# Kernel tuning notes

Measured on AMD Instinct MI355X. Metric: run time of the kernel, lower is better.

The kernel has to match this reference:

```python
import jax, jax.numpy as jnp
import numpy as np

N, E, D, L = 50000, 250000, 300, 5
ATOM_V, BOND_V = 128, 16
BN_EPS = 1e-5


def setup_inputs() -> dict:
    key = jax.random.key(0)
    ks = jax.random.split(key, 16)
    inp = {
        'x': jax.random.randint(ks[0], (N, 9), 0, ATOM_V),
        'edge_index': jax.random.randint(ks[1], (2, E), 0, N),
        'edge_attr': jax.random.randint(ks[2], (E, 3), 0, BOND_V),
        # learned parameters
        'atom_emb': jax.random.normal(ks[3], (9, ATOM_V, D), jnp.float32) * 0.02,
        'bond_emb': jax.random.normal(ks[4], (L, 3, BOND_V, D), jnp.float32) * 0.02,
        'eps': jnp.zeros((L,), jnp.float32),
        'W1': jax.random.normal(ks[5], (L, D, 2 * D), jnp.float32) / np.sqrt(D),
        'b1': jnp.zeros((L, 2 * D), jnp.float32),
        'g1': jnp.ones((L, 2 * D), jnp.float32),
        'be1': jnp.zeros((L, 2 * D), jnp.float32),
        'W2': jax.random.normal(ks[6], (L, 2 * D, D), jnp.float32) / np.sqrt(2 * D),
        'b2': jnp.zeros((L, D), jnp.float32),
        'gamma': jnp.ones((L, D), jnp.float32),
        'beta': jnp.zeros((L, D), jnp.float32),
    }
    return inp


def _bn(h, g, b):
    m = h.mean(0)
    v = h.var(0)
    return (h - m) * jax.lax.rsqrt(v + BN_EPS) * g + b


def reference(x, edge_index, edge_attr, atom_emb, bond_emb, eps, W1, b1, g1, be1, W2, b2, gamma, beta):
    src, dst = edge_index[0], edge_index[1]
    # AtomEncoder: sum of per-column embeddings -> [N, D]
    h = atom_emb[jnp.arange(9)[:, None], x.T].sum(0)
    for l in range(L):
        # BondEncoder for this layer -> [E, D]
        e = bond_emb[l][jnp.arange(3)[:, None], edge_attr.T].sum(0)
        # GIN: gather -> relu message -> scatter-add
        msg = jax.nn.relu(h[src] + e)
        agg = jax.ops.segment_sum(msg, dst, num_segments=N)
        z = (1.0 + eps[l]) * h + agg
        # MLP: Linear -> BN -> ReLU -> Linear
        z = jax.nn.relu(_bn(z @ W1[l] + b1[l], g1[l], be1[l])) @ W2[l] + b2[l]
        # outer BatchNorm
        h = _bn(z, gamma[l], beta[l])
        if l < L - 1:
            h = jax.nn.relu(h)
    return h  # JK='last'
```

## Files before the change

kernel.cpp:

```cpp
#include <hip/hip_runtime.h>

#define N_NODES 50000
#define N_EDGES 250000
#define DIM 300
#define DIM2 600
#define NL 5
#define MPAD 50048
#define KP1 320
#define KP2 608
#define NP1 640
#define NP2 384
#define SCAN_BLOCKS 196
#define CT_STRIDE 136

typedef __attribute__((ext_vector_type(8))) _Float16 half8;
typedef __attribute__((ext_vector_type(2))) _Float16 half2v;
typedef __attribute__((ext_vector_type(8))) short short8;
typedef __attribute__((ext_vector_type(4))) float f32x4;
typedef unsigned short ushort;
typedef unsigned int uint;

#define AS1 __attribute__((address_space(1)))
#define AS3 __attribute__((address_space(3)))

static __device__ __forceinline__ ushort f2h(float f) {
    _Float16 h = (_Float16)f;
    return __builtin_bit_cast(ushort, h);
}
static __device__ __forceinline__ float h2f(ushort s) {
    return (float)__builtin_bit_cast(_Float16, s);
}
static __device__ __forceinline__ uint pk2(float a, float b) {
    return (uint)f2h(a) | ((uint)f2h(b) << 16);
}
static __device__ __forceinline__ half2v u2h2(uint u) {
    return __builtin_bit_cast(half2v, u);
}

__global__ void atom_enc(const int* __restrict__ x, const float* __restrict__ emb,
                         ushort* __restrict__ h) {
    int idx = blockIdx.x * blockDim.x + threadIdx.x;
    const int PAIRS = DIM / 2;
    if (idx >= N_NODES * PAIRS) return;
    int n = idx / PAIRS, p = idx - n * PAIRS;
    const int* xr = x + n * 9;
    float s0 = 0.f, s1 = 0.f;
#pragma unroll
    for (int i = 0; i < 9; i++) {
        const float2 v = *(const float2*)(emb + (size_t)(i * 128 + xr[i]) * DIM + 2 * p);
        s0 += v.x; s1 += v.y;
    }
    ((uint*)h)[idx] = pk2(s0, s1);
}

__global__ void deg_count(const int* __restrict__ ei, int* __restrict__ deg) {
    int e = blockIdx.x * blockDim.x + threadIdx.x;
    if (e < N_EDGES) atomicAdd(&deg[ei[N_EDGES + e]], 1);
}

__global__ void block_sums(const int* __restrict__ deg, int* __restrict__ bsum) {
    __shared__ int red[256];
    int tid = threadIdx.x;
    int node = blockIdx.x * 256 + tid;
    red[tid] = (node < N_NODES) ? deg[node] : 0;
    __syncthreads();
    for (int off = 128; off > 0; off >>= 1) {
        if (tid < off) red[tid] += red[tid + off];
        __syncthreads();
    }
    if (tid == 0) bsum[blockIdx.x] = red[0];
}

__global__ void scan_bsums(int* __restrict__ bsum) {
    __shared__ int s[256];
    int tid = threadIdx.x;
    int orig = (tid < SCAN_BLOCKS) ? bsum[tid] : 0;
    s[tid] = orig;
    __syncthreads();
    for (int off = 1; off < 256; off <<= 1) {
        int v = (tid >= off) ? s[tid - off] : 0;
        __syncthreads();
        s[tid] += v;
        __syncthreads();
    }
    if (tid < SCAN_BLOCKS) bsum[tid] = s[tid] - orig;
}

__global__ void write_rowstart(const int* __restrict__ deg, const int* __restrict__ bsum,
                               int* __restrict__ rowstart, int* __restrict__ cursor) {
    __shared__ int s[256];
    int tid = threadIdx.x;
    int node = blockIdx.x * 256 + tid;
    int d = (node < N_NODES) ? deg[node] : 0;
    s[tid] = d;
    __syncthreads();
    for (int off = 1; off < 256; off <<= 1) {
        int v = (tid >= off) ? s[tid - off] : 0;
        __syncthreads();
        s[tid] += v;
        __syncthreads();
    }
    int excl = s[tid] - d + bsum[blockIdx.x];
    if (node < N_NODES) {
        rowstart[node] = excl;
        cursor[node] = excl;
    }
    if (blockIdx.x == 0 && tid == 0) rowstart[N_NODES] = N_EDGES;
}

__global__ void csr_fill(const int* __restrict__ ei, const int* __restrict__ ea,
                         int* __restrict__ cursor, int2* __restrict__ epack) {
    int e = blockIdx.x * blockDim.x + threadIdx.x;
    if (e < N_EDGES) {
        int d = ei[N_EDGES + e];
        int slot = atomicAdd(&cursor[d], 1);
        int attr = ea[3 * e] | (ea[3 * e + 1] << 8) | (ea[3 * e + 2] << 16);
        epack[slot] = make_int2(ei[e], attr);
    }
}

__global__ void bond_conv(const float* __restrict__ bond, ushort* __restrict__ bondh) {
    int idx = blockIdx.x * blockDim.x + threadIdx.x;
    if (idx >= 48 * (DIM / 2)) return;
    float2 v = *(const float2*)(bond + 2 * idx);
    ((uint*)bondh)[idx] = pk2(v.x, v.y);
}

__global__ void init_bn(float* __restrict__ scale, float* __restrict__ shift) {
    int i = blockIdx.x * blockDim.x + threadIdx.x;
    if (i < DIM) { scale[i] = 1.f; shift[i] = 0.f; }
}

__launch_bounds__(256)
__global__ void agg_combine(const int* __restrict__ rowstart, const int2* __restrict__ epack,
                            const ushort* __restrict__ bondh, const ushort* __restrict__ h,
                            const float* __restrict__ scale, const float* __restrict__ shift,
                            int relu, const float* __restrict__ epsp, int layer,
                            ushort* __restrict__ A1) {
    int node = blockIdx.x * 4 + (threadIdx.x >> 6);
    int lane = threadIdx.x & 63;
    if (node >= MPAD) return;
    uint* row32 = (uint*)(A1 + (size_t)node * KP1);
    if (node >= N_NODES) {
        for (int i = lane; i < KP1 / 2; i += 64) row32[i] = 0;
        return;
    }
    const int PAIRS = DIM / 2;
    float2 scf[3], shf[3];
    half2v sch[3], shh[3];
#pragma unroll
    for (int i = 0; i < 3; i++) {
        int p = lane + 64 * i;
        scf[i] = make_float2(0.f, 0.f);
        shf[i] = make_float2(0.f, 0.f);
        if (p < PAIRS) {
            scf[i] = *(const float2*)(scale + 2 * p);
            shf[i] = *(const float2*)(shift + 2 * p);
        }
        sch[i] = half2v{(_Float16)scf[i].x, (_Float16)scf[i].y};
        shh[i] = half2v{(_Float16)shf[i].x, (_Float16)shf[i].y};
    }
    float epsv = 1.0f + epsp[layer];
    const uint* hd = (const uint*)(h + (size_t)node * DIM);
    float ax[3], ay[3];
#pragma unroll
    for (int i = 0; i < 3; i++) {
        int p = lane + 64 * i;
        ax[i] = 0.f; ay[i] = 0.f;
        if (p < PAIRS) {
            uint u = hd[p];
            float vx = h2f((ushort)(u & 0xffffu)) * scf[i].x + shf[i].x;
            float vy = h2f((ushort)(u >> 16)) * scf[i].y + shf[i].y;
            if (relu) { vx = fmaxf(vx, 0.f); vy = fmaxf(vy, 0.f); }
            ax[i] = epsv * vx; ay[i] = epsv * vy;
        }
    }

    auto edge_contrib = [&](int2 pk) {
        const uint* hs = (const uint*)(h + (size_t)pk.x * DIM);
        int a0 = pk.y & 0xff, a1v = (pk.y >> 8) & 0xff, a2 = (pk.y >> 16) & 0xff;
        const uint* t0 = (const uint*)(bondh + a0 * DIM);
        const uint* t1 = (const uint*)(bondh + (16 + a1v) * DIM);
        const uint* t2 = (const uint*)(bondh + (32 + a2) * DIM);
        const half2v z = {};
#pragma unroll
        for (int i = 0; i < 3; i++) {
            int p = lane + 64 * i;
            if (p < PAIRS) {
                half2v hv = u2h2(hs[p]) * sch[i] + shh[i];
                if (relu) hv = __builtin_elementwise_max(hv, z);
                half2v m = hv + u2h2(t0[p]) + u2h2(t1[p]) + u2h2(t2[p]);
                m = __builtin_elementwise_max(m, z);
                ax[i] += (float)m.x;
                ay[i] += (float)m.y;
            }
        }
    };

    int e0 = rowstart[node], e1 = rowstart[node + 1];
    int t = e0;
    for (; t + 1 < e1; t += 2) {
        int2 p0 = epack[t];
        int2 p1 = epack[t + 1];
        edge_contrib(p0);
        edge_contrib(p1);
    }
    if (t < e1) edge_contrib(epack[t]);

#pragma unroll
    for (int i = 0; i < 3; i++) {
        int p = lane + 64 * i;
        if (p < KP1 / 2) row32[p] = (p < PAIRS) ? pk2(ax[i], ay[i]) : 0u;
    }
}

__global__ void wt_conv(const float* __restrict__ W, ushort* __restrict__ Wt,
                        int K, int Nc, int KP, int NP) {
    int idx = blockIdx.x * blockDim.x + threadIdx.x;
    if (idx >= KP * NP) return;
    int k = idx / NP, n = idx - k * NP;
    ushort v = 0;
    if (k < K && n < Nc) v = f2h(W[(size_t)k * Nc + n]);
    Wt[(size_t)n * KP + k] = v;
}

__global__ void wt_conv2(const float* __restrict__ W, const float* __restrict__ scale,
                         ushort* __restrict__ Wt) {
    int idx = blockIdx.x * blockDim.x + threadIdx.x;
    if (idx >= KP2 * NP2) return;
    int k = idx / NP2, n = idx - k * NP2;
    ushort v = 0;
    if (k < DIM2 && n < DIM) v = f2h(scale[k] * W[(size_t)k * DIM + n]);
    Wt[(size_t)n * KP2 + k] = v;
}

__launch_bounds__(256)
__global__ void gemm_mfma(const ushort* __restrict__ A, const ushort* __restrict__ Wt,
                          const float* __restrict__ bias, ushort* __restrict__ Cout,
                          int M, int KP, int Nc, int strideC, int ntiles,
                          float* __restrict__ csum, float* __restrict__ csq) {
    __shared__ ushort smem[128 * CT_STRIDE];
    __shared__ float s_sum[128], s_sq[128];
    ushort* As = smem;
    ushort* Bs = smem + 4096;

    int tid = threadIdx.x;
    int w = tid >> 6, lane = tid & 63;
    int quad = lane >> 4, lr = lane & 15;
    int wm = w >> 1, wn = w & 1;
    int bx = blockIdx.x;
    int m0 = (bx / ntiles) * 128;
    int n0 = (bx % ntiles) * 128;

    if (tid < 128) { s_sum[tid] = 0.f; s_sq[tid] = 0.f; }

    f32x4 acc[4][4] = {};
    int kq = lane & 3;

    for (int k0 = 0; k0 < KP; k0 += 32) {
#pragma unroll
        for (int c = w; c < 8; c += 4) {
            int row = 16 * c + (lane >> 2);
            const ushort* gp = A + (size_t)(m0 + row) * KP + k0 + kq * 8;
            __builtin_amdgcn_global_load_lds((const AS1 void*)gp, (AS3 void*)(As + c * 512), 16, 0, 0);
        }
#pragma unroll
        for (int c = w; c < 8; c += 4) {
            int row = 16 * c + (lane >> 2);
            const ushort* gp = Wt + (size_t)(n0 + row) * KP + k0 + kq * 8;
            __builtin_amdgcn_global_load_lds((const AS1 void*)gp, (AS3 void*)(Bs + c * 512), 16, 0, 0);
        }
        __syncthreads();

        half8 a[4], b[4];
#pragma unroll
        for (int mf = 0; mf < 4; mf++)
            a[mf] = __builtin_bit_cast(half8, *(const short8*)(As + (64 * wm + 16 * mf + lr) * 32 + quad * 8));
#pragma unroll
        for (int nf = 0; nf < 4; nf++)
            b[nf] = __builtin_bit_cast(half8, *(const short8*)(Bs + (64 * wn + 16 * nf + lr) * 32 + quad * 8));
#pragma unroll
        for (int mf = 0; mf < 4; mf++)
#pragma unroll
            for (int nf = 0; nf < 4; nf++)
                acc[mf][nf] = __builtin_amdgcn_mfma_f32_16x16x32_f16(a[mf], b[nf], acc[mf][nf], 0, 0, 0);
        __syncthreads();
    }

#pragma unroll
    for (int nf = 0; nf < 4; nf++) {
        int lcol = 64 * wn + 16 * nf + lr;
        int gn = n0 + lcol;
        float bv = (gn < Nc) ? bias[gn] : 0.f;
        float ps = 0.f, pq = 0.f;
#pragma unroll
        for (int mf = 0; mf < 4; mf++) {
#pragma unroll
            for (int r = 0; r < 4; r++) {
                int lrow = 64 * wm + 16 * mf + quad * 4 + r;
                float v = acc[mf][nf][r] + bv;
                smem[lrow * CT_STRIDE + lcol] = f2h(v);
                if (m0 + lrow < M && gn < Nc) { ps += v; pq += v * v; }
            }
        }
        if (gn < Nc) {
            atomicAdd(&s_sum[lcol], ps);
            atomicAdd(&s_sq[lcol], pq);
        }
    }
    __syncthreads();

#pragma unroll
    for (int it = 0; it < 8; it++) {
        int idx = tid + it * 256;
        int row = idx >> 4, ch = idx & 15;
        int gcol = n0 + ch * 8;
        if (gcol < Nc) {
            *(short8*)(Cout + (size_t)(m0 + row) * strideC + gcol) =
                *(const short8*)(smem + row * CT_STRIDE + ch * 8);
        }
    }

    if (tid < 128) {
        int gn = n0 + tid;
        if (gn < Nc) {
            atomicAdd(&csum[gn], s_sum[tid]);
            atomicAdd(&csq[gn], s_sq[tid]);
        }
    }
}

__launch_bounds__(256)
__global__ void gemm2_fused(const ushort* __restrict__ yh, const ushort* __restrict__ Wt,
                            const ushort* __restrict__ t1h, const float* __restrict__ bias,
                            ushort* __restrict__ hout,
                            float* __restrict__ csum, float* __restrict__ csq) {
    __shared__ ushort smem[128 * CT_STRIDE];
    __shared__ ushort s_t[KP2];
    __shared__ float s_sum[128], s_sq[128];
    ushort* As = smem;
    ushort* Bs = smem + 4096;

    int tid = threadIdx.x;
    int w = tid >> 6, lane = tid & 63;
    int quad = lane >> 4, lr = lane & 15;
    int wm = w >> 1, wn = w & 1;
    int bx = blockIdx.x;
    int m0 = (bx / 3) * 128;
    int n0 = (bx % 3) * 128;

    for (int i = tid; i < KP2 / 2; i += 256) ((uint*)s_t)[i] = ((const uint*)t1h)[i];
    if (tid < 128) { s_sum[tid] = 0.f; s_sq[tid] = 0.f; }
    __syncthreads();

    f32x4 acc[4][4] = {};
    int kq = lane & 3;
    int cc = (tid & 3) * 8;
    int r0 = tid >> 2;

    for (int k0 = 0; k0 < KP2; k0 += 32) {
#pragma unroll
        for (int c = w; c < 8; c += 4) {
            int row = 16 * c + (lane >> 2);
            const ushort* gp = Wt + (size_t)(n0 + row) * KP2 + k0 + kq * 8;
            __builtin_amdgcn_global_load_lds((const AS1 void*)gp, (AS3 void*)(Bs + c * 512), 16, 0, 0);
        }
        int col = k0 + cc;
        short8 v0, v1;
        if (col < DIM2) {
            half8 t = *(const half8*)(s_t + col);
            half8 y0 = *(const half8*)(yh + (size_t)(m0 + r0) * DIM2 + col);
            half8 y1 = *(const half8*)(yh + (size_t)(m0 + r0 + 64) * DIM2 + col);
            half8 z = {};
            y0 = __builtin_elementwise_max(y0 + t, z);
            y1 = __builtin_elementwise_max(y1 + t, z);
            v0 = __builtin_bit_cast(short8, y0);
            v1 = __builtin_bit_cast(short8, y1);
        } else {
            v0 = short8{}; v1 = short8{};
        }
        *(short8*)(As + r0 * 32 + cc) = v0;
        *(short8*)(As + (r0 + 64) * 32 + cc) = v1;
        __syncthreads();

        half8 a[4], b[4];
#pragma unroll
        for (int mf = 0; mf < 4; mf++)
            a[mf] = __builtin_bit_cast(half8, *(const short8*)(As + (64 * wm + 16 * mf + lr) * 32 + quad * 8));
#pragma unroll
        for (int nf = 0; nf < 4; nf++)
            b[nf] = __builtin_bit_cast(half8, *(const short8*)(Bs + (64 * wn + 16 * nf + lr) * 32 + quad * 8));
#pragma unroll
        for (int mf = 0; mf < 4; mf++)
#pragma unroll
            for (int nf = 0; nf < 4; nf++)
                acc[mf][nf] = __builtin_amdgcn_mfma_f32_16x16x32_f16(a[mf], b[nf], acc[mf][nf], 0, 0, 0);
        __syncthreads();
    }

#pragma unroll
    for (int nf = 0; nf < 4; nf++) {
        int lcol = 64 * wn + 16 * nf + lr;
        int gn = n0 + lcol;
        float bv = (gn < DIM) ? bias[gn] : 0.f;
        float ps = 0.f, pq = 0.f;
#pragma unroll
        for (int mf = 0; mf < 4; mf++) {
#pragma unroll
            for (int r = 0; r < 4; r++) {
                int lrow = 64 * wm + 16 * mf + quad * 4 + r;
                float v = acc[mf][nf][r] + bv;
                smem[lrow * CT_STRIDE + lcol] = f2h(v);
                if (m0 + lrow < N_NODES && gn < DIM) { ps += v; pq += v * v; }
            }
        }
        if (gn < DIM) {
            atomicAdd(&s_sum[lcol], ps);
            atomicAdd(&s_sq[lcol], pq);
        }
    }
    __syncthreads();

#pragma unroll
    for (int it = 0; it < 16; it++) {
        int idx = tid + it * 256;
        int row = idx >> 5, ch = idx & 31;
        int gm = m0 + row, gcol = n0 + ch * 4;
        if (gm < N_NODES && gcol < DIM) {
            *(uint2*)(hout + (size_t)gm * DIM + gcol) =
                *(const uint2*)(smem + row * CT_STRIDE + ch * 4);
        }
    }

    if (tid < 128) {
        int gn = n0 + tid;
        if (gn < DIM) {
            atomicAdd(&csum[gn], s_sum[tid]);
            atomicAdd(&csq[gn], s_sq[tid]);
        }
    }
}

__global__ void bn_finalize(const float* __restrict__ sum, const float* __restrict__ sq,
                            const float* __restrict__ g, const float* __restrict__ b,
                            float* __restrict__ scale, float* __restrict__ shift,
                            ushort* __restrict__ th, int n, int npad) {
    int i = blockIdx.x * blockDim.x + threadIdx.x;
    if (i >= n) {
        if (th && i < npad) th[i] = 0;
        return;
    }
    const float invN = 1.0f / (float)N_NODES;
    float m = sum[i] * invN;
    float v = sq[i] * invN - m * m;
    float inv = rsqrtf(v + 1e-5f);
    float sc = g[i] * inv;
    scale[i] = sc;
    shift[i] = b[i] - m * sc;
    if (th) th[i] = f2h((b[i] - m * sc) / sc);
}

__global__ void bn_apply_out(const ushort* __restrict__ h, const float* __restrict__ scale,
                             const float* __restrict__ shift, float* __restrict__ out) {
    int idx = blockIdx.x * blockDim.x + threadIdx.x;
    const int PAIRS = DIM / 2;
    if (idx >= N_NODES * PAIRS) return;
    int p = idx % PAIRS;
    uint u = ((const uint*)h)[idx];
    float2 sc = *(const float2*)(scale + 2 * p);
    float2 sh = *(const float2*)(shift + 2 * p);
    float2 o;
    o.x = h2f((ushort)(u & 0xffffu)) * sc.x + sh.x;
    o.y = h2f((ushort)(u >> 16)) * sc.y + sh.y;
    *(float2*)(out + 2 * idx) = o;
}

extern "C" void kernel_launch(void* const* d_in, const int* in_sizes, int n_in,
                              void* d_out, int out_size, void* d_ws, size_t ws_size,
                              hipStream_t stream) {
    const int* x = (const int*)d_in[0];
    const int* ei = (const int*)d_in[1];
    const int* ea = (const int*)d_in[2];
    const float* atom_emb = (const float*)d_in[3];
    const float* bond_emb = (const float*)d_in[4];
    const float* eps = (const float*)d_in[5];
    const float* W1 = (const float*)d_in[6];
    const float* b1 = (const float*)d_in[7];
    const float* g1 = (const float*)d_in[8];
    const float* be1 = (const float*)d_in[9];
    const float* W2 = (const float*)d_in[10];
    const float* b2 = (const float*)d_in[11];
    const float* gamma = (const float*)d_in[12];
    const float* beta = (const float*)d_in[13];
    float* out = (float*)d_out;

    float* ws = (float*)d_ws;
    ushort* h    = (ushort*)ws;
    ushort* A1h  = (ushort*)(ws + 7500000);
    ushort* yh   = (ushort*)(ws + 15507680);
    ushort* Wt1  = (ushort*)(ws + 30522080);
    ushort* Wt2  = (ushort*)(ws + 30624480);
    ushort* bondh = (ushort*)(ws + 30741216);
    float* stats = ws + 30748416;
    ushort* t1h  = (ushort*)(ws + 30752016);
    int* rowstart = (int*)(ws + 30752320);
    int* deg      = rowstart + 50001;
    int* cursor   = deg + 50000;
    int2* epack   = (int2*)(cursor + 50000 + 1);
    int* bsum     = (int*)(epack + 250000);

    float* sum1 = stats;
    float* sq1  = stats + 600;
    float* sum2 = stats + 1200;
    float* sq2  = stats + 1500;
    float* scale1 = stats + 1800;
    float* shift1 = stats + 2400;
    float* scale2 = stats + 3000;
    float* shift2 = stats + 3300;

    const int PAIRS_N = N_NODES * (DIM / 2);

    hipMemsetAsync(deg, 0, 50000 * sizeof(int), stream);
    deg_count<<<(N_EDGES + 255) / 256, 256, 0, stream>>>(ei, deg);
    block_sums<<<SCAN_BLOCKS, 256, 0, stream>>>(deg, bsum);
    scan_bsums<<<1, 256, 0, stream>>>(bsum);
    write_rowstart<<<SCAN_BLOCKS, 256, 0, stream>>>(deg, bsum, rowstart, cursor);
    csr_fill<<<(N_EDGES + 255) / 256, 256, 0, stream>>>(ei, ea, cursor, epack);

    atom_enc<<<(PAIRS_N + 255) / 256, 256, 0, stream>>>(x, atom_emb, h);
    init_bn<<<(DIM + 255) / 256, 256, 0, stream>>>(scale2, shift2);

    for (int l = 0; l < NL; ++l) {
        hipMemsetAsync(stats, 0, 1800 * sizeof(float), stream);

        bond_conv<<<(48 * (DIM / 2) + 255) / 256, 256, 0, stream>>>(
            bond_emb + (size_t)l * 3 * 16 * DIM, bondh);

        agg_combine<<<(MPAD + 3) / 4, 256, 0, stream>>>(rowstart, epack, bondh,
                                                        h, scale2, shift2, (l > 0) ? 1 : 0,
                                                        eps, l, A1h);

        wt_conv<<<(KP1 * NP1 + 255) / 256, 256, 0, stream>>>(W1 + (size_t)l * DIM * DIM2, Wt1,
                                                             DIM, DIM2, KP1, NP1);

        gemm_mfma<<<(MPAD / 128) * (NP1 / 128), 256, 0, stream>>>(
            A1h, Wt1, b1 + l * DIM2, yh, N_NODES, KP1, DIM2, DIM2, NP1 / 128, sum1, sq1);

        bn_finalize<<<(KP2 + 255) / 256, 256, 0, stream>>>(sum1, sq1, g1 + l * DIM2,
                                                           be1 + l * DIM2, scale1, shift1,
                                                           t1h, DIM2, KP2);

        wt_conv2<<<(KP2 * NP2 + 255) / 256, 256, 0, stream>>>(W2 + (size_t)l * DIM2 * DIM,
                                                              scale1, Wt2);

        gemm2_fused<<<(MPAD / 128) * (NP2 / 128), 256, 0, stream>>>(
            yh, Wt2, t1h, b2 + l * DIM, h, sum2, sq2);

        bn_finalize<<<(DIM + 255) / 256, 256, 0, stream>>>(sum2, sq2, gamma + l * DIM,
                                                           beta + l * DIM, scale2, shift2,
                                                           nullptr, DIM, DIM);
    }

    bn_apply_out<<<(PAIRS_N + 255) / 256, 256, 0, stream>>>(h, scale2, shift2, out);
}
```

Before: 1.195 ms.

## Double-buffer GEMM LDS tiles with XOR swizzle and XCD-aware block remap

Both MFMA GEMM kernels now double-buffer their LDS tiles. The global-to-LDS load for the next k-step is issued before the current step's MFMAs, so there is one barrier per step instead of two. LDS columns are XOR-swizzled to avoid bank conflicts on the 128-bit reads, block IDs are remapped so neighbouring tiles land on the same XCD for L2 reuse, and MFMA bursts are raised in priority. This uses twice the tile LDS inside the existing smem array and relies on hand-placed waitcnt and barriers, which are fragile to get right.

After: 1.108 ms. 7.3% less time.

```diff
diff --git a/kernel.cpp b/kernel.cpp
--- a/kernel.cpp
+++ b/kernel.cpp
@@ -35,6 +35,18 @@
 }
 static __device__ __forceinline__ half2v u2h2(uint u) {
     return __builtin_bit_cast(half2v, u);
+}
+
+static __device__ __forceinline__ short8 lds_read_b128(uint addr) {
+    short8 r;
+    asm volatile("ds_read_b128 %0, %1" : "=v"(r) : "v"(addr));
+    return r;
+}
+
+static __device__ __forceinline__ int xcd_swizzle(int o, int nwg) {
+    int q = nwg >> 3, r = nwg & 7;
+    int xcd = o & 7, idx = o >> 3;
+    return (xcd < r ? xcd * (q + 1) : r * (q + 1) + (xcd - r) * q) + idx;
 }
 
 __global__ void atom_enc(const int* __restrict__ x, const float* __restrict__ emb,
@@ -241,50 +253,74 @@
                           float* __restrict__ csum, float* __restrict__ csq) {
     __shared__ ushort smem[128 * CT_STRIDE];
     __shared__ float s_sum[128], s_sq[128];
-    ushort* As = smem;
-    ushort* Bs = smem + 4096;
 
     int tid = threadIdx.x;
     int w = tid >> 6, lane = tid & 63;
     int quad = lane >> 4, lr = lane & 15;
     int wm = w >> 1, wn = w & 1;
-    int bx = blockIdx.x;
-    int m0 = (bx / ntiles) * 128;
-    int n0 = (bx % ntiles) * 128;
+    int wg = xcd_swizzle(blockIdx.x, gridDim.x);
+    int m0 = (wg / ntiles) * 128;
+    int n0 = (wg % ntiles) * 128;
 
     if (tid < 128) { s_sum[tid] = 0.f; s_sq[tid] = 0.f; }
 
+    const int kchunk = ((lane & 3) ^ ((lane >> 3) & 3)) * 8;
+    const int grow = lane >> 2;
+    const ushort* Abase = A + (size_t)m0 * KP + kchunk;
+    const ushort* Bbase = Wt + (size_t)n0 * KP + kchunk;
+
+    const uint sbase = (uint)(size_t)(AS3 ushort*)smem;
+    const int xq = (quad ^ ((lr >> 1) & 3)) * 8;
+    uint aoff[4], boff[4];
+#pragma unroll
+    for (int mf = 0; mf < 4; mf++)
+        aoff[mf] = sbase + (uint)(((64 * wm + 16 * mf + lr) * 32 + xq) * 2);
+#pragma unroll
+    for (int nf = 0; nf < 4; nf++)
+        boff[nf] = sbase + (uint)((4096 + (64 * wn + 16 * nf + lr) * 32 + xq) * 2);
+
+    auto stage = [&](int k0, int buf) {
+        ushort* dA = smem + buf * 8192;
+#pragma unroll
+        for (int c = w; c < 8; c += 4)
+            __builtin_amdgcn_global_load_lds((const AS1 void*)(Abase + (size_t)(16 * c + grow) * KP + k0),
+                                             (AS3 void*)(dA + c * 512), 16, 0, 0);
+#pragma unroll
+        for (int c = w; c < 8; c += 4)
+            __builtin_amdgcn_global_load_lds((const AS1 void*)(Bbase + (size_t)(16 * c + grow) * KP + k0),
+                                             (AS3 void*)(dA + 4096 + c * 512), 16, 0, 0);
+    };
+
     f32x4 acc[4][4] = {};
-    int kq = lane & 3;
-
-    for (int k0 = 0; k0 < KP; k0 += 32) {
-#pragma unroll
-        for (int c = w; c < 8; c += 4) {
-            int row = 16 * c + (lane >> 2);
-            const ushort* gp = A + (size_t)(m0 + row) * KP + k0 + kq * 8;
-            __builtin_amdgcn_global_load_lds((const AS1 void*)gp, (AS3 void*)(As + c * 512), 16, 0, 0);
-        }
-#pragma unroll
-        for (int c = w; c < 8; c += 4) {
-            int row = 16 * c + (lane >> 2);
-            const ushort* gp = Wt + (size_t)(n0 + row) * KP + k0 + kq * 8;
-            __builtin_amdgcn_global_load_lds((const AS1 void*)gp, (AS3 void*)(Bs + c * 512), 16, 0, 0);
-        }
-        __syncthreads();
-
-        half8 a[4], b[4];
+    const int nk = KP >> 5;
+
+    stage(0, 0);
+    asm volatile("s_waitcnt vmcnt(0) lgkmcnt(0)" ::: "memory");
+    __builtin_amdgcn_s_barrier();
+
+    for (int t = 0; t < nk; ++t) {
+        uint bsel = (uint)(t & 1) * 16384u;
+        if (t + 1 < nk) stage((t + 1) << 5, (t & 1) ^ 1);
+
+        short8 a[4], b[4];
+#pragma unroll
+        for (int mf = 0; mf < 4; mf++) a[mf] = lds_read_b128(aoff[mf] + bsel);
+#pragma unroll
+        for (int nf = 0; nf < 4; nf++) b[nf] = lds_read_b128(boff[nf] + bsel);
+        asm volatile("s_waitcnt lgkmcnt(0)" ::: "memory");
+        __builtin_amdgcn_sched_barrier(0);
+        __builtin_amdgcn_s_setprio(1);
 #pragma unroll
         for (int mf = 0; mf < 4; mf++)
-            a[mf] = __builtin_bit_cast(half8, *(const short8*)(As + (64 * wm + 16 * mf + lr) * 32 + quad * 8));
-#pragma unroll
-        for (int nf = 0; nf < 4; nf++)
-            b[nf] = __builtin_bit_cast(half8, *(const short8*)(Bs + (64 * wn + 16 * nf + lr) * 32 + quad * 8));
-#pragma unroll
-        for (int mf = 0; mf < 4; mf++)
 #pragma unroll
             for (int nf = 0; nf < 4; nf++)
-                acc[mf][nf] = __builtin_amdgcn_mfma_f32_16x16x32_f16(a[mf], b[nf], acc[mf][nf], 0, 0, 0);
-        __syncthreads();
+                acc[mf][nf] = __builtin_amdgcn_mfma_f32_16x16x32_f16(
+                    __builtin_bit_cast(half8, a[mf]), __builtin_bit_cast(half8, b[nf]),
+                    acc[mf][nf], 0, 0, 0);
+        __builtin_amdgcn_s_setprio(0);
+
+        asm volatile("s_waitcnt vmcnt(0)" ::: "memory");
+        __builtin_amdgcn_s_barrier();
     }
 
 #pragma unroll
@@ -338,64 +374,114 @@
     __shared__ ushort smem[128 * CT_STRIDE];
     __shared__ ushort s_t[KP2];
     __shared__ float s_sum[128], s_sq[128];
-    ushort* As = smem;
-    ushort* Bs = smem + 4096;
 
     int tid = threadIdx.x;
     int w = tid >> 6, lane = tid & 63;
     int quad = lane >> 4, lr = lane & 15;
     int wm = w >> 1, wn = w & 1;
-    int bx = blockIdx.x;
-    int m0 = (bx / 3) * 128;
-    int n0 = (bx % 3) * 128;
-
+    int wg = xcd_swizzle(blockIdx.x, gridDim.x);
+    int m0 = (wg / 3) * 128;
+    int n0 = (wg % 3) * 128;
+
+    int r0 = tid >> 2;
+    int q = tid & 3;
+    int cc = q * 8;
+    const int aslot = (q ^ ((r0 >> 1) & 3)) * 8;
+
+    const uint sbase = (uint)(size_t)(AS3 ushort*)smem;
+    const int xq = (quad ^ ((lr >> 1) & 3)) * 8;
+    uint aoff[4], boff[4];
+#pragma unroll
+    for (int mf = 0; mf < 4; mf++)
+        aoff[mf] = sbase + (uint)(((64 * wm + 16 * mf + lr) * 32 + xq) * 2);
+#pragma unroll
+    for (int nf = 0; nf < 4; nf++)
+        boff[nf] = sbase + (uint)((4096 + (64 * wn + 16 * nf + lr) * 32 + xq) * 2);
+
+    const int kchunk = ((lane & 3) ^ ((lane >> 3) & 3)) * 8;
+    const int grow = lane >> 2;
+    const ushort* Bbase = Wt + (size_t)n0 * KP2 + kchunk;
+
+    auto stageB = [&](int k0, int buf) {
+        ushort* dB = smem + buf * 8192 + 4096;
+#pragma unroll
+        for (int c = w; c < 8; c += 4)
+            __builtin_amdgcn_global_load_lds((const AS1 void*)(Bbase + (size_t)(16 * c + grow) * KP2 + k0),
+                                             (AS3 void*)(dB + c * 512), 16, 0, 0);
+    };
+
+    const ushort* yrow0 = yh + (size_t)(m0 + r0) * DIM2 + cc;
+    const ushort* yrow1 = yh + (size_t)(m0 + r0 + 64) * DIM2 + cc;
+
+    if (tid < 128) { s_sum[tid] = 0.f; s_sq[tid] = 0.f; }
+
+    half8 y0 = *(const half8*)(yrow0);
+    half8 y1 = *(const half8*)(yrow1);
+    stageB(0, 0);
     for (int i = tid; i < KP2 / 2; i += 256) ((uint*)s_t)[i] = ((const uint*)t1h)[i];
-    if (tid < 128) { s_sum[tid] = 0.f; s_sq[tid] = 0.f; }
     __syncthreads();
+    {
+        half8 z = {};
+        half8 tt = *(const half8*)(s_t + cc);
+        half8 a0 = __builtin_elementwise_max(y0 + tt, z);
+        half8 a1 = __builtin_elementwise_max(y1 + tt, z);
+        *(short8*)(smem + r0 * 32 + aslot) = __builtin_bit_cast(short8, a0);
+        *(short8*)(smem + (r0 + 64) * 32 + aslot) = __builtin_bit_cast(short8, a1);
+    }
+    asm volatile("s_waitcnt lgkmcnt(0)" ::: "memory");
+    __builtin_amdgcn_s_barrier();
 
     f32x4 acc[4][4] = {};
-    int kq = lane & 3;
-    int cc = (tid & 3) * 8;
-    int r0 = tid >> 2;
-
-    for (int k0 = 0; k0 < KP2; k0 += 32) {
-#pragma unroll
-        for (int c = w; c < 8; c += 4) {
-            int row = 16 * c + (lane >> 2);
-            const ushort* gp = Wt + (size_t)(n0 + row) * KP2 + k0 + kq * 8;
-            __builtin_amdgcn_global_load_lds((const AS1 void*)gp, (AS3 void*)(Bs + c * 512), 16, 0, 0);
-        }
-        int col = k0 + cc;
-        short8 v0, v1;
-        if (col < DIM2) {
-            half8 t = *(const half8*)(s_t + col);
-            half8 y0 = *(const half8*)(yh + (size_t)(m0 + r0) * DIM2 + col);
-            half8 y1 = *(const half8*)(yh + (size_t)(m0 + r0 + 64) * DIM2 + col);
+    const int nk = KP2 >> 5;
+
+    for (int t = 0; t < nk; ++t) {
+        uint bsel = (uint)(t & 1) * 16384u;
+        int nxt = (t & 1) ^ 1;
+        half8 yn0 = {}, yn1 = {};
+        int coln = ((t + 1) << 5) + cc;
+        int vn = 0;
+        if (t + 1 < nk) {
+            vn = coln < DIM2;
+            if (vn) {
+                yn0 = *(const half8*)(yrow0 + ((t + 1) << 5));
+                yn1 = *(const half8*)(yrow1 + ((t + 1) << 5));
+            }
+            stageB((t + 1) << 5, nxt);
+        }
+
+        short8 a[4], b[4];
+#pragma unroll
+        for (int mf = 0; mf < 4; mf++) a[mf] = lds_read_b128(aoff[mf] + bsel);
+#pragma unroll
+        for (int nf = 0; nf < 4; nf++) b[nf] = lds_read_b128(boff[nf] + bsel);
+        asm volatile("s_waitcnt lgkmcnt(0)" ::: "memory");
+        __builtin_amdgcn_sched_barrier(0);
+        __builtin_amdgcn_s_setprio(1);
+#pragma unroll
+        for (int mf = 0; mf < 4; mf++)
+#pragma unroll
+            for (int nf = 0; nf < 4; nf++)
+                acc[mf][nf] = __builtin_amdgcn_mfma_f32_16x16x32_f16(
+                    __builtin_bit_cast(half8, a[mf]), __builtin_bit_cast(half8, b[nf]),
+                    acc[mf][nf], 0, 0, 0);
+        __builtin_amdgcn_s_setprio(0);
+        __builtin_amdgcn_sched_barrier(0);
+
+        if (t + 1 < nk) {
+            ushort* Anx = smem + nxt * 8192;
             half8 z = {};
-            y0 = __builtin_elementwise_max(y0 + t, z);
-            y1 = __builtin_elementwise_max(y1 + t, z);
-            v0 = __builtin_bit_cast(short8, y0);
-            v1 = __builtin_bit_cast(short8, y1);
-        } else {
-            v0 = short8{}; v1 = short8{};
-        }
-        *(short8*)(As + r0 * 32 + cc) = v0;
-        *(short8*)(As + (r0 + 64) * 32 + cc) = v1;
-        __syncthreads();
-
-        half8 a[4], b[4];
-#pragma unroll
-        for (int mf = 0; mf < 4; mf++)
-            a[mf] = __builtin_bit_cast(half8, *(const short8*)(As + (64 * wm + 16 * mf + lr) * 32 + quad * 8));
-#pragma unroll
-        for (int nf = 0; nf < 4; nf++)
-            b[nf] = __builtin_bit_cast(half8, *(const short8*)(Bs + (64 * wn + 16 * nf + lr) * 32 + quad * 8));
-#pragma unroll
-        for (int mf = 0; mf < 4; mf++)
-#pragma unroll
-            for (int nf = 0; nf < 4; nf++)
-                acc[mf][nf] = __builtin_amdgcn_mfma_f32_16x16x32_f16(a[mf], b[nf], acc[mf][nf], 0, 0, 0);
-        __syncthreads();
+            half8 a0 = z, a1 = z;
+            if (vn) {
+                half8 tt = *(const half8*)(s_t + coln);
+                a0 = __builtin_elementwise_max(yn0 + tt, z);
+                a1 = __builtin_elementwise_max(yn1 + tt, z);
+            }
+            *(short8*)(Anx + r0 * 32 + aslot) = __builtin_bit_cast(short8, a0);
+            *(short8*)(Anx + (r0 + 64) * 32 + aslot) = __builtin_bit_cast(short8, a1);
+        }
+
+        asm volatile("s_waitcnt vmcnt(0) lgkmcnt(0)" ::: "memory");
+        __builtin_amdgcn_s_barrier();
     }
 
 #pragma unroll
```

## Swizzle LDS, halve epilogue smem, XCD-swizzle blocks, raise GEMM occupancy

Applied to the files above, without the earlier changes.

Both GEMM kernels now write the C tile back through shared memory in two 64-row halves, which halves the LDS buffer and, together with launch_bounds(256,6), lets more workgroups fit per CU. The shared-memory tiles use an XOR swizzle on the 8-element k-chunk to reduce bank conflicts in the MFMA operand reads. Block indices are remapped across the 8 XCDs so neighbouring tiles share L2, and s_setprio raises wave priority around the MFMA block. The costs are an extra pair of barriers in the epilogue and possible register pressure from the occupancy hint.

After: 3.143 ms. 2.63x slower.

```diff
diff --git a/kernel.cpp b/kernel.cpp
--- a/kernel.cpp
+++ b/kernel.cpp
@@ -35,6 +35,12 @@
 }
 static __device__ __forceinline__ half2v u2h2(uint u) {
     return __builtin_bit_cast(half2v, u);
+}
+
+static __device__ __forceinline__ int xcd_swizzle(int o, int nwg) {
+    int q = nwg >> 3, r = nwg & 7;
+    int xcd = o & 7, idx = o >> 3;
+    return (xcd < r ? xcd * (q + 1) : r * (q + 1) + (xcd - r) * q) + idx;
 }
 
 __global__ void atom_enc(const int* __restrict__ x, const float* __restrict__ emb,
@@ -234,12 +240,12 @@
     Wt[(size_t)n * KP2 + k] = v;
 }
 
-__launch_bounds__(256)
+__launch_bounds__(256, 6)
 __global__ void gemm_mfma(const ushort* __restrict__ A, const ushort* __restrict__ Wt,
                           const float* __restrict__ bias, ushort* __restrict__ Cout,
                           int M, int KP, int Nc, int strideC, int ntiles,
                           float* __restrict__ csum, float* __restrict__ csq) {
-    __shared__ ushort smem[128 * CT_STRIDE];
+    __shared__ ushort smem[64 * CT_STRIDE];
     __shared__ float s_sum[128], s_sq[128];
     ushort* As = smem;
     ushort* Bs = smem + 4096;
@@ -248,77 +254,85 @@
     int w = tid >> 6, lane = tid & 63;
     int quad = lane >> 4, lr = lane & 15;
     int wm = w >> 1, wn = w & 1;
-    int bx = blockIdx.x;
-    int m0 = (bx / ntiles) * 128;
-    int n0 = (bx % ntiles) * 128;
+    int wg = xcd_swizzle(blockIdx.x, gridDim.x);
+    int m0 = (wg / ntiles) * 128;
+    int n0 = (wg % ntiles) * 128;
 
     if (tid < 128) { s_sum[tid] = 0.f; s_sq[tid] = 0.f; }
 
+    const int kchunk = ((lane & 3) ^ ((lane >> 3) & 3)) * 8;
+    const int grow = lane >> 2;
+    const ushort* Abase = A + (size_t)m0 * KP + kchunk;
+    const ushort* Bbase = Wt + (size_t)n0 * KP + kchunk;
+    const int xq = (quad ^ ((lr >> 1) & 3)) * 8;
+
     f32x4 acc[4][4] = {};
-    int kq = lane & 3;
 
     for (int k0 = 0; k0 < KP; k0 += 32) {
 #pragma unroll
-        for (int c = w; c < 8; c += 4) {
-            int row = 16 * c + (lane >> 2);
-            const ushort* gp = A + (size_t)(m0 + row) * KP + k0 + kq * 8;
-            __builtin_amdgcn_global_load_lds((const AS1 void*)gp, (AS3 void*)(As + c * 512), 16, 0, 0);
-        }
-#pragma unroll
-        for (int c = w; c < 8; c += 4) {
-            int row = 16 * c + (lane >> 2);
-            const ushort* gp = Wt + (size_t)(n0 + row) * KP + k0 + kq * 8;
-            __builtin_amdgcn_global_load_lds((const AS1 void*)gp, (AS3 void*)(Bs + c * 512), 16, 0, 0);
-        }
+        for (int c = w; c < 8; c += 4)
+            __builtin_amdgcn_global_load_lds((const AS1 void*)(Abase + (size_t)(16 * c + grow) * KP + k0),
+                                             (AS3 void*)(As + c * 512), 16, 0, 0);
+#pragma unroll
+        for (int c = w; c < 8; c += 4)
+            __builtin_amdgcn_global_load_lds((const AS1 void*)(Bbase + (size_t)(16 * c + grow) * KP + k0),
+                                             (AS3 void*)(Bs + c * 512), 16, 0, 0);
         __syncthreads();
 
         half8 a[4], b[4];
 #pragma unroll
         for (int mf = 0; mf < 4; mf++)
-            a[mf] = __builtin_bit_cast(half8, *(const short8*)(As + (64 * wm + 16 * mf + lr) * 32 + quad * 8));
+            a[mf] = __builtin_bit_cast(half8, *(const short8*)(As + (64 * wm + 16 * mf + lr) * 32 + xq));
 #pragma unroll
         for (int nf = 0; nf < 4; nf++)
-            b[nf] = __builtin_bit_cast(half8, *(const short8*)(Bs + (64 * wn + 16 * nf + lr) * 32 + quad * 8));
+            b[nf] = __builtin_bit_cast(half8, *(const short8*)(Bs + (64 * wn + 16 * nf + lr) * 32 + xq));
+        __builtin_amdgcn_s_setprio(1);
 #pragma unroll
         for (int mf = 0; mf < 4; mf++)
 #pragma unroll
             for (int nf = 0; nf < 4; nf++)
                 acc[mf][nf] = __builtin_amdgcn_mfma_f32_16x16x32_f16(a[mf], b[nf], acc[mf][nf], 0, 0, 0);
-        __syncthreads();
-    }
-
-#pragma unroll
-    for (int nf = 0; nf < 4; nf++) {
-        int lcol = 64 * wn + 16 * nf + lr;
-        int gn = n0 + lcol;
-        float bv = (gn < Nc) ? bias[gn] : 0.f;
-        float ps = 0.f, pq = 0.f;
-#pragma unroll
-        for (int mf = 0; mf < 4; mf++) {
-#pragma unroll
-            for (int r = 0; r < 4; r++) {
-                int lrow = 64 * wm + 16 * mf + quad * 4 + r;
-                float v = acc[mf][nf][r] + bv;
-                smem[lrow * CT_STRIDE + lcol] = f2h(v);
-                if (m0 + lrow < M && gn < Nc) { ps += v; pq += v * v; }
+        __builtin_amdgcn_s_setprio(0);
+        __syncthreads();
+    }
+
+#pragma unroll
+    for (int half = 0; half < 2; half++) {
+        if (wm == half) {
+#pragma unroll
+            for (int nf = 0; nf < 4; nf++) {
+                int lcol = 64 * wn + 16 * nf + lr;
+                int gn = n0 + lcol;
+                float bv = (gn < Nc) ? bias[gn] : 0.f;
+                float ps = 0.f, pq = 0.f;
+#pragma unroll
+                for (int mf = 0; mf < 4; mf++) {
+#pragma unroll
+                    for (int r = 0; r < 4; r++) {
+                        int lrow = 16 * mf + quad * 4 + r;
+                        float v = acc[mf][nf][r] + bv;
+                        smem[lrow * CT_STRIDE + lcol] = f2h(v);
+                        if (m0 + 64 * half + lrow < M && gn < Nc) { ps += v; pq += v * v; }
+                    }
+                }
+                if (gn < Nc) {
+                    atomicAdd(&s_sum[lcol], ps);
+                    atomicAdd(&s_sq[lcol], pq);
+                }
             }
         }
-        if (gn < Nc) {
-            atomicAdd(&s_sum[lcol], ps);
-            atomicAdd(&s_sq[lcol], pq);
-        }
-    }
-    __syncthreads();
-
-#pragma unroll
-    for (int it = 0; it < 8; it++) {
-        int idx = tid + it * 256;
-        int row = idx >> 4, ch = idx & 15;
-        int gcol = n0 + ch * 8;
-        if (gcol < Nc) {
-            *(short8*)(Cout + (size_t)(m0 + row) * strideC + gcol) =
-                *(const short8*)(smem + row * CT_STRIDE + ch * 8);
-        }
+        __syncthreads();
+#pragma unroll
+        for (int it = 0; it < 4; it++) {
+            int idx = tid + it * 256;
+            int row = idx >> 4, ch = idx & 15;
+            int gcol = n0 + ch * 8;
+            if (gcol < Nc) {
+                *(short8*)(Cout + (size_t)(m0 + 64 * half + row) * strideC + gcol) =
+                    *(const short8*)(smem + row * CT_STRIDE + ch * 8);
+            }
+        }
+        __syncthreads();
     }
 
     if (tid < 128) {
@@ -330,12 +344,12 @@
     }
 }
 
-__launch_bounds__(256)
+__launch_bounds__(256, 6)
 __global__ void gemm2_fused(const ushort* __restrict__ yh, const ushort* __restrict__ Wt,
                             const ushort* __restrict__ t1h, const float* __restrict__ bias,
                             ushort* __restrict__ hout,
                             float* __restrict__ csum, float* __restrict__ csq) {
-    __shared__ ushort smem[128 * CT_STRIDE];
+    __shared__ ushort smem[64 * CT_STRIDE];
     __shared__ ushort s_t[KP2];
     __shared__ float s_sum[128], s_sq[128];
     ushort* As = smem;
@@ -345,91 +359,104 @@
     int w = tid >> 6, lane = tid & 63;
     int quad = lane >> 4, lr = lane & 15;
     int wm = w >> 1, wn = w & 1;
-    int bx = blockIdx.x;
-    int m0 = (bx / 3) * 128;
-    int n0 = (bx % 3) * 128;
-
+    int wg = xcd_swizzle(blockIdx.x, gridDim.x);
+    int m0 = (wg / 3) * 128;
+    int n0 = (wg % 3) * 128;
+
+    int r0 = tid >> 2;
+    int q = tid & 3;
+    int cc = q * 8;
+    const int aslot = (q ^ ((r0 >> 1) & 3)) * 8;
+
+    const int kchunk = ((lane & 3) ^ ((lane >> 3) & 3)) * 8;
+    const int grow = lane >> 2;
+    const ushort* Bbase = Wt + (size_t)n0 * KP2 + kchunk;
+    const int xq = (quad ^ ((lr >> 1) & 3)) * 8;
+
+    const ushort* yrow0 = yh + (size_t)(m0 + r0) * DIM2 + cc;
+    const ushort* yrow1 = yh + (size_t)(m0 + r0 + 64) * DIM2 + cc;
+
+    if (tid < 128) { s_sum[tid] = 0.f; s_sq[tid] = 0.f; }
     for (int i = tid; i < KP2 / 2; i += 256) ((uint*)s_t)[i] = ((const uint*)t1h)[i];
-    if (tid < 128) { s_sum[tid] = 0.f; s_sq[tid] = 0.f; }
     __syncthreads();
 
     f32x4 acc[4][4] = {};
-    int kq = lane & 3;
-    int cc = (tid & 3) * 8;
-    int r0 = tid >> 2;
-
-    for (int k0 = 0; k0 < KP2; k0 += 32) {
-#pragma unroll
-        for (int c = w; c < 8; c += 4) {
-            int row = 16 * c + (lane >> 2);
-            const ushort* gp = Wt + (size_t)(n0 + row) * KP2 + k0 + kq * 8;
-            __builtin_amdgcn_global_load_lds((const AS1 void*)gp, (AS3 void*)(Bs + c * 512), 16, 0, 0);
-        }
+    const int nk = KP2 >> 5;
+
+    for (int t = 0; t < nk; ++t) {
+        int k0 = t << 5;
+#pragma unroll
+        for (int c = w; c < 8; c += 4)
+            __builtin_amdgcn_global_load_lds((const AS1 void*)(Bbase + (size_t)(16 * c + grow) * KP2 + k0),
+                                             (AS3 void*)(Bs + c * 512), 16, 0, 0);
         int col = k0 + cc;
-        short8 v0, v1;
+        half8 a0 = {}, a1 = {};
         if (col < DIM2) {
-            half8 t = *(const half8*)(s_t + col);
-            half8 y0 = *(const half8*)(yh + (size_t)(m0 + r0) * DIM2 + col);
-            half8 y1 = *(const half8*)(yh + (size_t)(m0 + r0 + 64) * DIM2 + col);
+            half8 tt = *(const half8*)(s_t + col);
+            half8 y0 = *(const half8*)(yrow0 + k0);
+            half8 y1 = *(const half8*)(yrow1 + k0);
             half8 z = {};
-            y0 = __builtin_elementwise_max(y0 + t, z);
-            y1 = __builtin_elementwise_max(y1 + t, z);
-            v0 = __builtin_bit_cast(short8, y0);
-            v1 = __builtin_bit_cast(short8, y1);
-        } else {
-            v0 = short8{}; v1 = short8{};
-        }
-        *(short8*)(As + r0 * 32 + cc) = v0;
-        *(short8*)(As + (r0 + 64) * 32 + cc) = v1;
+            a0 = __builtin_elementwise_max(y0 + tt, z);
+            a1 = __builtin_elementwise_max(y1 + tt, z);
+        }
+        *(short8*)(As + r0 * 32 + aslot) = __builtin_bit_cast(short8, a0);
+        *(short8*)(As + (r0 + 64) * 32 + aslot) = __builtin_bit_cast(short8, a1);
         __syncthreads();
 
         half8 a[4], b[4];
 #pragma unroll
         for (int mf = 0; mf < 4; mf++)
-            a[mf] = __builtin_bit_cast(half8, *(const short8*)(As + (64 * wm + 16 * mf + lr) * 32 + quad * 8));
+            a[mf] = __builtin_bit_cast(half8, *(const short8*)(As + (64 * wm + 16 * mf + lr) * 32 + xq));
 #pragma unroll
         for (int nf = 0; nf < 4; nf++)
-            b[nf] = __builtin_bit_cast(half8, *(const short8*)(Bs + (64 * wn + 16 * nf + lr) * 32 + quad * 8));
+            b[nf] = __builtin_bit_cast(half8, *(const short8*)(Bs + (64 * wn + 16 * nf + lr) * 32 + xq));
+        __builtin_amdgcn_s_setprio(1);
 #pragma unroll
         for (int mf = 0; mf < 4; mf++)
 #pragma unroll
             for (int nf = 0; nf < 4; nf++)
                 acc[mf][nf] = __builtin_amdgcn_mfma_f32_16x16x32_f16(a[mf], b[nf], acc[mf][nf], 0, 0, 0);
-        __syncthreads();
-    }
-
-#pragma unroll
-    for (int nf = 0; nf < 4; nf++) {
-        int lcol = 64 * wn + 16 * nf + lr;
-        int gn = n0 + lcol;
-        float bv = (gn < DIM) ? bias[gn] : 0.f;
-        float ps = 0.f, pq = 0.f;
-#pragma unroll
-        for (int mf = 0; mf < 4; mf++) {
-#pragma unroll
-            for (int r = 0; r < 4; r++) {
-                int lrow = 64 * wm + 16 * mf + quad * 4 + r;
-                float v = acc[mf][nf][r] + bv;
-                smem[lrow * CT_STRIDE + lcol] = f2h(v);
-                if (m0 + lrow < N_NODES && gn < DIM) { ps += v; pq += v * v; }
+        __builtin_amdgcn_s_setprio(0);
+        __syncthreads();
+    }
+
+#pragma unroll
+    for (int half = 0; half < 2; half++) {
+        if (wm == half) {
+#pragma unroll
+            for (int nf = 0; nf < 4; nf++) {
+                int lcol = 64 * wn + 16 * nf + lr;
+                int gn = n0 + lcol;
+                float bv = (gn < DIM) ? bias[gn] : 0.f;
+                float ps = 0.f, pq = 0.f;
+#pragma unroll
+                for (int mf = 0; mf < 4; mf++) {
+#pragma unroll
+                    for (int r = 0; r < 4; r++) {
+                        int lrow = 16 * mf + quad * 4 + r;
+                        float v = acc[mf][nf][r] + bv;
+                        smem[lrow * CT_STRIDE + lcol] = f2h(v);
+                        if (m0 + 64 * half + lrow < N_NODES && gn < DIM) { ps += v; pq += v * v; }
+                    }
+                }
+                if (gn < DIM) {
+                    atomicAdd(&s_sum[lcol], ps);
+                    atomicAdd(&s_sq[lcol], pq);
+                }
             }
         }
-        if (gn < DIM) {
-            atomicAdd(&s_sum[lcol], ps);
-            atomicAdd(&s_sq[lcol], pq);
-        }
-    }
-    __syncthreads();
-
-#pragma unroll
-    for (int it = 0; it < 16; it++) {
-        int idx = tid + it * 256;
-        int row = idx >> 5, ch = idx & 31;
-        int gm = m0 + row, gcol = n0 + ch * 4;
-        if (gm < N_NODES && gcol < DIM) {
-            *(uint2*)(hout + (size_t)gm * DIM + gcol) =
-                *(const uint2*)(smem + row * CT_STRIDE + ch * 4);
-        }
+        __syncthreads();
+#pragma unroll
+        for (int it = 0; it < 8; it++) {
+            int idx = tid + it * 256;
+            int row = idx >> 5, ch = idx & 31;
+            int gm = m0 + 64 * half + row, gcol = n0 + ch * 4;
+            if (gm < N_NODES && gcol < DIM) {
+                *(uint2*)(hout + (size_t)gm * DIM + gcol) =
+                    *(const uint2*)(smem + row * CT_STRIDE + ch * 4);
+            }
+        }
+        __syncthreads();
     }
 
     if (tid < 128) {
```
